# Performance work log

Hardware: AMD Instinct MI355X
Metric: run time of the kernel (lower is better)

## Reference

```python
import jax, jax.numpy as jnp
import numpy as np

NUM_STREAM = 4
SINKHORN_ITERS = 20
HC_EPS = 1e-06
NORM_EPS = 1e-06


def sinkhorn_knopps(h, iters, eps):
    # h: [B, S, ns, ns]
    h = jax.nn.softmax(h, axis=-1) + eps
    h = h / (h.sum(-2, keepdims=True) + eps)
    for _ in range(iters - 1):  # fixed small trip count (19), unrolled
        h = h / (h.sum(-1, keepdims=True) + eps)
        h = h / (h.sum(-2, keepdims=True) + eps)
    return h


def setup_inputs() -> dict:
    key = jax.random.key(0)
    k1, k2, k3, k4 = jax.random.split(key, 4)
    B, S, ns, H = 4, 2048, NUM_STREAM, 1024
    mix_hc = (2 + ns) * ns  # 24
    x = jax.random.normal(k1, (B, S, ns, H), dtype=jnp.float32)
    hc_fn = jax.random.normal(k2, (mix_hc, ns * H), dtype=jnp.float32) * 0.02
    hc_scale = jax.random.uniform(k3, (3,), dtype=jnp.float32)
    hc_base = jax.random.normal(k4, (mix_hc,), dtype=jnp.float32)
    return {"x": x, "hc_fn": hc_fn, "hc_scale": hc_scale, "hc_base": hc_base}


def reference(x, hc_fn, hc_scale, hc_base):
    B, S, ns, H = x.shape
    xf = x.reshape(B, S, ns * H).astype(jnp.float32)
    # RMSNorm stats (applied as a post-scale on the linear output, as in source)
    rsqrt = jax.lax.rsqrt(jnp.mean(jnp.square(xf), axis=-1, keepdims=True) + NORM_EPS)
    weight = jnp.einsum('bsd,md->bsm', xf, hc_fn) * rsqrt  # [B, S, mix_hc]
    h_pre = weight[..., :ns]
    h_post = weight[..., ns:2 * ns]
    h_res = weight[..., 2 * ns:].reshape(B, S, ns, ns)
    h_pre = jax.nn.sigmoid(h_pre * hc_scale[0] + hc_base[:ns][None, None, :]) + HC_EPS
    h_post = 2.0 * jax.nn.sigmoid(h_post * hc_scale[1] + hc_base[ns:2 * ns][None, None, :])
    h_res = h_res * hc_scale[2] + hc_base[2 * ns:].reshape(ns, ns)[None, None, :, :]
    h_res = sinkhorn_knopps(h_res, SINKHORN_ITERS, HC_EPS)
    xs = xf.reshape(B, S, ns, H)
    # hc_pre: mix streams into a single vector per token
    y = jnp.einsum('bsn,bsnh->bsh', h_pre, xs)  # [B, S, H]
    # hc_post: broadcast gated y back to streams + Sinkhorn-mixed residual streams
    out = h_post[..., None] * y[:, :, None, :] + jnp.einsum('bsij,bsih->bsjh', h_res, xs)
    return out.astype(x.dtype)
```

## Files before the change

kernel.cpp:

```cpp
#include <hip/hip_runtime.h>
#include <math.h>

#define NS 4
#define HDIM 1024
#define DDIM 4096
#define TOK_B 32
#define KCH 512
#define NPS 16
#define HC_EPS_F 1e-6f
#define NORM_EPS_F 1e-6f

typedef __attribute__((ext_vector_type(8))) short short8;
typedef __attribute__((ext_vector_type(4))) float f32x4;

__device__ __forceinline__ float frcp(float v) { return __builtin_amdgcn_rcpf(v); }

__device__ __forceinline__ void gload_lds16(const float* g, float* l) {
  __builtin_amdgcn_global_load_lds(
      (const __attribute__((address_space(1))) void*)g,
      (__attribute__((address_space(3))) void*)l, 16, 0, 0);
}

#define CVT_PAIR(j, f0, f1)                                                     \
  { unsigned p0 = __float_as_uint(f0), p1 = __float_as_uint(f1);                \
    H.u[j] = (p1 & 0xFFFF0000u) | (p0 >> 16);                                   \
    unsigned q0 = __float_as_uint((f0) - __uint_as_float(p0 & 0xFFFF0000u));    \
    unsigned q1 = __float_as_uint((f1) - __uint_as_float(p1 & 0xFFFF0000u));    \
    L.u[j] = (q1 & 0xFFFF0000u) | (q0 >> 16); }

__device__ __forceinline__ void cvt_hl(const float4 a, const float4 b,
                                       short8& hi, short8& lo) {
  union { unsigned u[4]; short8 s; } H, L;
  CVT_PAIR(0, a.x, a.y)
  CVT_PAIR(1, a.z, a.w)
  CVT_PAIR(2, b.x, b.y)
  CVT_PAIR(3, b.z, b.w)
  hi = H.s; lo = L.s;
}

__launch_bounds__(256, 2)
__global__ void mhc_dots_mfma(const float* __restrict__ x,
                              const float* __restrict__ hc_fn,
                              float* __restrict__ wp, int ntok) {
  __shared__ float xs[TOK_B * KCH];
  const int tid  = threadIdx.x;
  const int lane = tid & 63;
  const int wave = tid >> 6;
  const int mt = blockIdx.x >> 3;
  const int kc = blockIdx.x & 7;
  const long long tok0 = (long long)mt * TOK_B;
  const int k0 = kc * KCH;

  #pragma unroll
  for (int c = 0; c < 16; ++c) {
    const int S = c * 256 + wave * 64;
    const int t = S >> 7;
    const int b = (S & 127) + lane;
    gload_lds16(x + (tok0 + t) * DDIM + k0 + b * 4, xs + (size_t)S * 4);
  }

  const int th = wave & 1;
  const int kh = wave >> 1;
  const int row = lane & 15;
  const int ks  = lane >> 4;

  const float4* bp0 = (const float4*)(hc_fn + (long long)row * DDIM + k0 + kh * 256) + ks * 2;
  const int fr1c = (row < 8) ? (16 + row) : 23;
  const float4* bp1 = (const float4*)(hc_fn + (long long)fr1c * DDIM + k0 + kh * 256) + ks * 2;
  const bool v1 = (row < 8);
  const float4 z4 = {0.f, 0.f, 0.f, 0.f};

  f32x4 acc0 = {0.f, 0.f, 0.f, 0.f};
  f32x4 acc1 = {0.f, 0.f, 0.f, 0.f};
  float ssq = 0.f;

  float4 b00_c = bp0[0], b01_c = bp0[1];
  float4 b10_c = v1 ? bp1[0] : z4, b11_c = v1 ? bp1[1] : z4;

  __syncthreads();

  const float* a_base = xs + (size_t)(th * 16 + row) * KCH + kh * 256 + ks * 8;

  #pragma unroll
  for (int s = 0; s < 8; ++s) {
    float4 b00_n, b01_n, b10_n, b11_n;
    if (s < 7) {
      const int o = (s + 1) * 8;
      b00_n = bp0[o]; b01_n = bp0[o + 1];
      b10_n = v1 ? bp1[o] : z4; b11_n = v1 ? bp1[o + 1] : z4;
    }
    const float4 a0 = *(const float4*)(a_base + s * 32);
    const float4 a1 = *(const float4*)(a_base + s * 32 + 4);

    ssq = fmaf(a0.x, a0.x, fmaf(a0.y, a0.y, fmaf(a0.z, a0.z, fmaf(a0.w, a0.w, ssq))));
    ssq = fmaf(a1.x, a1.x, fmaf(a1.y, a1.y, fmaf(a1.z, a1.z, fmaf(a1.w, a1.w, ssq))));

    short8 ahi, alo, b0hi, b0lo, b1hi, b1lo;
    cvt_hl(a0, a1, ahi, alo);
    cvt_hl(b00_c, b01_c, b0hi, b0lo);
    cvt_hl(b10_c, b11_c, b1hi, b1lo);

    acc0 = __builtin_amdgcn_mfma_f32_16x16x32_bf16(ahi, b0hi, acc0, 0, 0, 0);
    acc1 = __builtin_amdgcn_mfma_f32_16x16x32_bf16(ahi, b1hi, acc1, 0, 0, 0);
    acc0 = __builtin_amdgcn_mfma_f32_16x16x32_bf16(ahi, b0lo, acc0, 0, 0, 0);
    acc1 = __builtin_amdgcn_mfma_f32_16x16x32_bf16(ahi, b1lo, acc1, 0, 0, 0);
    acc0 = __builtin_amdgcn_mfma_f32_16x16x32_bf16(alo, b0hi, acc0, 0, 0, 0);
    acc1 = __builtin_amdgcn_mfma_f32_16x16x32_bf16(alo, b1hi, acc1, 0, 0, 0);

    if (s < 7) {
      b00_c = b00_n; b01_c = b01_n;
      b10_c = b10_n; b11_c = b11_n;
    }
  }

  ssq += __shfl_xor(ssq, 16, 64);
  ssq += __shfl_xor(ssq, 32, 64);

  const int ps = kc * 2 + kh;
  float* wpk = wp + (long long)ps * ntok * 25;
  const long long tbase = tok0 + th * 16;
  if (lane < 16) wpk[(tbase + lane) * 25 + 24] = ssq;
  const int rq = lane >> 4;
  #pragma unroll
  for (int r = 0; r < 4; ++r)
    wpk[(tbase + rq * 4 + r) * 25 + row] = acc0[r];
  if (row < 8) {
    #pragma unroll
    for (int r = 0; r < 4; ++r)
      wpk[(tbase + rq * 4 + r) * 25 + 16 + row] = acc1[r];
  }
}

__launch_bounds__(256, 4)
__global__ void mhc_sinkhorn(const float* __restrict__ wp,
                             const float* __restrict__ hc_scale,
                             const float* __restrict__ hc_base,
                             float* __restrict__ gates, int ntok) {
  const int lane = threadIdx.x & 63;
  const int wave = threadIdx.x >> 6;
  const long long tok = (long long)blockIdx.x * 16 + wave * 4 + (lane >> 4);
  const int e = lane & 15;

  const long long kstride = (long long)ntok * 25;
  const float* b = wp + tok * 25;
  float sres = 0.f, ssq = 0.f, spre = 0.f, spost = 0.f;
  #pragma unroll
  for (int ps = 0; ps < NPS; ++ps) {
    const float* p = b + ps * kstride;
    sres += p[8 + e];
    ssq  += p[24];
    if (e < NS) { spre += p[e]; spost += p[NS + e]; }
  }

  const float rs = rsqrtf(ssq * (1.0f / DDIM) + NORM_EPS_F);
  const float s0 = hc_scale[0], s1 = hc_scale[1], s2 = hc_scale[2];

  float h = sres * rs * s2 + hc_base[8 + e];
  float mx = fmaxf(h, __shfl_xor(h, 1, 4));
  mx = fmaxf(mx, __shfl_xor(mx, 2, 4));
  float ex = expf(h - mx);
  float sm = ex + __shfl_xor(ex, 1, 4);
  sm += __shfl_xor(sm, 2, 4);
  h = ex * frcp(sm) + HC_EPS_F;
  float cs = h + __shfl_xor(h, 4, 16);
  cs += __shfl_xor(cs, 8, 16);
  h *= frcp(cs + HC_EPS_F);
  #pragma unroll 1
  for (int itn = 0; itn < 19; ++itn) {
    float rsum = h + __shfl_xor(h, 1, 4);
    rsum += __shfl_xor(rsum, 2, 4);
    h *= frcp(rsum + HC_EPS_F);
    float csum = h + __shfl_xor(h, 4, 16);
    csum += __shfl_xor(csum, 8, 16);
    h *= frcp(csum + HC_EPS_F);
  }
  float* g = gates + tok * 24;
  g[8 + e] = h;
  if (e < NS) {
    g[e] = frcp(1.0f + expf(-(spre * rs * s0 + hc_base[e]))) + HC_EPS_F;
    g[NS + e] = 2.0f * frcp(1.0f + expf(-(spost * rs * s1 + hc_base[NS + e])));
  }
}

__launch_bounds__(256, 8)
__global__ void mhc_out(const float* __restrict__ x,
                        const float* __restrict__ gates,
                        float* __restrict__ out) {
  const long long token = blockIdx.x;
  const int q = threadIdx.x;

  const float* g = gates + token * 24;
  float hp[NS], hq[NS], hr[NS][NS];
  #pragma unroll
  for (int i = 0; i < NS; ++i) {
    hp[i] = g[i];
    hq[i] = g[NS + i];
    #pragma unroll
    for (int j = 0; j < NS; ++j) hr[i][j] = g[8 + i * NS + j];
  }

  const float4* xb = (const float4*)(x + token * DDIM);
  float4 xv[NS];
  #pragma unroll
  for (int i = 0; i < NS; ++i) xv[i] = xb[i * 256 + q];

  float4 y;
  y.x = hp[0]*xv[0].x + hp[1]*xv[1].x + hp[2]*xv[2].x + hp[3]*xv[3].x;
  y.y = hp[0]*xv[0].y + hp[1]*xv[1].y + hp[2]*xv[2].y + hp[3]*xv[3].y;
  y.z = hp[0]*xv[0].z + hp[1]*xv[1].z + hp[2]*xv[2].z + hp[3]*xv[3].z;
  y.w = hp[0]*xv[0].w + hp[1]*xv[1].w + hp[2]*xv[2].w + hp[3]*xv[3].w;

  float4* ob = (float4*)(out + token * DDIM);
  #pragma unroll
  for (int n = 0; n < NS; ++n) {
    float4 o;
    o.x = hq[n]*y.x + hr[0][n]*xv[0].x + hr[1][n]*xv[1].x + hr[2][n]*xv[2].x + hr[3][n]*xv[3].x;
    o.y = hq[n]*y.y + hr[0][n]*xv[0].y + hr[1][n]*xv[1].y + hr[2][n]*xv[2].y + hr[3][n]*xv[3].y;
    o.z = hq[n]*y.z + hr[0][n]*xv[0].z + hr[1][n]*xv[1].z + hr[2][n]*xv[2].z + hr[3][n]*xv[3].z;
    o.w = hq[n]*y.w + hr[0][n]*xv[0].w + hr[1][n]*xv[1].w + hr[2][n]*xv[2].w + hr[3][n]*xv[3].w;
    ob[n * 256 + q] = o;
  }
}

extern "C" void kernel_launch(void* const* d_in, const int* in_sizes, int n_in,
                              void* d_out, int out_size, void* d_ws, size_t ws_size,
                              hipStream_t stream) {
  const float* x        = (const float*)d_in[0];
  const float* hc_fn    = (const float*)d_in[1];
  const float* hc_scale = (const float*)d_in[2];
  const float* hc_base  = (const float*)d_in[3];
  float* out = (float*)d_out;

  const int ntok = in_sizes[0] / DDIM;
  float* gates = (float*)d_ws;
  float* wp    = out;

  mhc_dots_mfma<<<(ntok / TOK_B) * 8, 256, 0, stream>>>(x, hc_fn, wp, ntok);
  mhc_sinkhorn<<<ntok / 16, 256, 0, stream>>>(wp, hc_scale, hc_base, gates, ntok);
  mhc_out<<<ntok, 256, 0, stream>>>(x, gates, out);
}
```

Baseline: 99.84 us.

## Pre-split hc_fn into bf16 hi/lo once, shrink token tile, swizzle LDS

Adds a small kernel that converts hc_fn into bf16 hi and lo arrays once per call, so the dots kernel no longer repeats that conversion per block. The dots kernel now uses 16-token tiles with four waves splitting K, which doubles the block count and the number of K partials the Sinkhorn kernel reduces (NPS 32). The LDS layout is XOR-swizzled to reduce bank conflicts. The costs are an extra launch, twice as much partial-sum traffic through the output buffer, and the converted weights stored in the output scratch area.

```diff
diff --git a/kernel.cpp b/kernel.cpp
--- a/kernel.cpp
+++ b/kernel.cpp
@@ -4,9 +4,9 @@
 #define NS 4
 #define HDIM 1024
 #define DDIM 4096
-#define TOK_B 32
+#define TOK_B 16
 #define KCH 512
-#define NPS 16
+#define NPS 32
 #define HC_EPS_F 1e-6f
 #define NORM_EPS_F 1e-6f
 
@@ -38,9 +38,26 @@
   hi = H.s; lo = L.s;
 }
 
+__launch_bounds__(256, 4)
+__global__ void mhc_convb(const float* __restrict__ hc_fn,
+                          unsigned short* __restrict__ bh,
+                          unsigned short* __restrict__ bl) {
+  const int g = blockIdx.x * 256 + threadIdx.x;
+  const float4 v = ((const float4*)hc_fn)[g];
+  ushort4 h, l;
+  unsigned p;
+  p = __float_as_uint(v.x); h.x = p >> 16; l.x = __float_as_uint(v.x - __uint_as_float(p & 0xFFFF0000u)) >> 16;
+  p = __float_as_uint(v.y); h.y = p >> 16; l.y = __float_as_uint(v.y - __uint_as_float(p & 0xFFFF0000u)) >> 16;
+  p = __float_as_uint(v.z); h.z = p >> 16; l.z = __float_as_uint(v.z - __uint_as_float(p & 0xFFFF0000u)) >> 16;
+  p = __float_as_uint(v.w); h.w = p >> 16; l.w = __float_as_uint(v.w - __uint_as_float(p & 0xFFFF0000u)) >> 16;
+  ((ushort4*)bh)[g] = h;
+  ((ushort4*)bl)[g] = l;
+}
+
 __launch_bounds__(256, 2)
 __global__ void mhc_dots_mfma(const float* __restrict__ x,
-                              const float* __restrict__ hc_fn,
+                              const unsigned short* __restrict__ bh,
+                              const unsigned short* __restrict__ bl,
                               float* __restrict__ wp, int ntok) {
   __shared__ float xs[TOK_B * KCH];
   const int tid  = threadIdx.x;
@@ -52,82 +69,86 @@
   const int k0 = kc * KCH;
 
   #pragma unroll
-  for (int c = 0; c < 16; ++c) {
+  for (int c = 0; c < 8; ++c) {
     const int S = c * 256 + wave * 64;
     const int t = S >> 7;
-    const int b = (S & 127) + lane;
-    gload_lds16(x + (tok0 + t) * DDIM + k0 + b * 4, xs + (size_t)S * 4);
-  }
-
-  const int th = wave & 1;
-  const int kh = wave >> 1;
+    const int c4src = (((wave & 1) * 64 + lane) ^ (t & 7));
+    gload_lds16(x + (tok0 + t) * DDIM + k0 + c4src * 4, xs + (size_t)S * 4);
+  }
+
+  const int kh  = wave;
   const int row = lane & 15;
   const int ks  = lane >> 4;
 
-  const float4* bp0 = (const float4*)(hc_fn + (long long)row * DDIM + k0 + kh * 256) + ks * 2;
+  const unsigned short* bp0h = bh + (long long)row * DDIM + k0 + kh * 128 + ks * 8;
+  const unsigned short* bp0l = bl + (long long)row * DDIM + k0 + kh * 128 + ks * 8;
   const int fr1c = (row < 8) ? (16 + row) : 23;
-  const float4* bp1 = (const float4*)(hc_fn + (long long)fr1c * DDIM + k0 + kh * 256) + ks * 2;
+  const unsigned short* bp1h = bh + (long long)fr1c * DDIM + k0 + kh * 128 + ks * 8;
+  const unsigned short* bp1l = bl + (long long)fr1c * DDIM + k0 + kh * 128 + ks * 8;
   const bool v1 = (row < 8);
-  const float4 z4 = {0.f, 0.f, 0.f, 0.f};
+  const short8 z8 = {0, 0, 0, 0, 0, 0, 0, 0};
 
   f32x4 acc0 = {0.f, 0.f, 0.f, 0.f};
   f32x4 acc1 = {0.f, 0.f, 0.f, 0.f};
   float ssq = 0.f;
 
-  float4 b00_c = bp0[0], b01_c = bp0[1];
-  float4 b10_c = v1 ? bp1[0] : z4, b11_c = v1 ? bp1[1] : z4;
+  short8 b0h_c = *(const short8*)bp0h;
+  short8 b0l_c = *(const short8*)bp0l;
+  short8 b1h_c = v1 ? *(const short8*)bp1h : z8;
+  short8 b1l_c = v1 ? *(const short8*)bp1l : z8;
 
   __syncthreads();
 
-  const float* a_base = xs + (size_t)(th * 16 + row) * KCH + kh * 256 + ks * 8;
-
-  #pragma unroll
-  for (int s = 0; s < 8; ++s) {
-    float4 b00_n, b01_n, b10_n, b11_n;
-    if (s < 7) {
-      const int o = (s + 1) * 8;
-      b00_n = bp0[o]; b01_n = bp0[o + 1];
-      b10_n = v1 ? bp1[o] : z4; b11_n = v1 ? bp1[o + 1] : z4;
+  const int rsw = row & 7;
+  const float* arow = xs + (size_t)row * KCH;
+
+  #pragma unroll
+  for (int s = 0; s < 4; ++s) {
+    short8 b0h_n, b0l_n, b1h_n, b1l_n;
+    if (s < 3) {
+      const int o = (s + 1) * 32;
+      b0h_n = *(const short8*)(bp0h + o);
+      b0l_n = *(const short8*)(bp0l + o);
+      b1h_n = v1 ? *(const short8*)(bp1h + o) : z8;
+      b1l_n = v1 ? *(const short8*)(bp1l + o) : z8;
     }
-    const float4 a0 = *(const float4*)(a_base + s * 32);
-    const float4 a1 = *(const float4*)(a_base + s * 32 + 4);
+    const int c4 = kh * 32 + s * 8 + ks * 2;
+    const float4 a0 = *(const float4*)(arow + (size_t)(c4 ^ rsw) * 4);
+    const float4 a1 = *(const float4*)(arow + (size_t)((c4 + 1) ^ rsw) * 4);
 
     ssq = fmaf(a0.x, a0.x, fmaf(a0.y, a0.y, fmaf(a0.z, a0.z, fmaf(a0.w, a0.w, ssq))));
     ssq = fmaf(a1.x, a1.x, fmaf(a1.y, a1.y, fmaf(a1.z, a1.z, fmaf(a1.w, a1.w, ssq))));
 
-    short8 ahi, alo, b0hi, b0lo, b1hi, b1lo;
+    short8 ahi, alo;
     cvt_hl(a0, a1, ahi, alo);
-    cvt_hl(b00_c, b01_c, b0hi, b0lo);
-    cvt_hl(b10_c, b11_c, b1hi, b1lo);
-
-    acc0 = __builtin_amdgcn_mfma_f32_16x16x32_bf16(ahi, b0hi, acc0, 0, 0, 0);
-    acc1 = __builtin_amdgcn_mfma_f32_16x16x32_bf16(ahi, b1hi, acc1, 0, 0, 0);
-    acc0 = __builtin_amdgcn_mfma_f32_16x16x32_bf16(ahi, b0lo, acc0, 0, 0, 0);
-    acc1 = __builtin_amdgcn_mfma_f32_16x16x32_bf16(ahi, b1lo, acc1, 0, 0, 0);
-    acc0 = __builtin_amdgcn_mfma_f32_16x16x32_bf16(alo, b0hi, acc0, 0, 0, 0);
-    acc1 = __builtin_amdgcn_mfma_f32_16x16x32_bf16(alo, b1hi, acc1, 0, 0, 0);
-
-    if (s < 7) {
-      b00_c = b00_n; b01_c = b01_n;
-      b10_c = b10_n; b11_c = b11_n;
+
+    acc0 = __builtin_amdgcn_mfma_f32_16x16x32_bf16(ahi, b0h_c, acc0, 0, 0, 0);
+    acc1 = __builtin_amdgcn_mfma_f32_16x16x32_bf16(ahi, b1h_c, acc1, 0, 0, 0);
+    acc0 = __builtin_amdgcn_mfma_f32_16x16x32_bf16(ahi, b0l_c, acc0, 0, 0, 0);
+    acc1 = __builtin_amdgcn_mfma_f32_16x16x32_bf16(ahi, b1l_c, acc1, 0, 0, 0);
+    acc0 = __builtin_amdgcn_mfma_f32_16x16x32_bf16(alo, b0h_c, acc0, 0, 0, 0);
+    acc1 = __builtin_amdgcn_mfma_f32_16x16x32_bf16(alo, b1h_c, acc1, 0, 0, 0);
+
+    if (s < 3) {
+      b0h_c = b0h_n; b0l_c = b0l_n;
+      b1h_c = b1h_n; b1l_c = b1l_n;
     }
   }
 
   ssq += __shfl_xor(ssq, 16, 64);
   ssq += __shfl_xor(ssq, 32, 64);
 
-  const int ps = kc * 2 + kh;
+  const int ps = kc * 4 + kh;
   float* wpk = wp + (long long)ps * ntok * 25;
-  const long long tbase = tok0 + th * 16;
-  if (lane < 16) wpk[(tbase + lane) * 25 + 24] = ssq;
+  if (lane < 16) wpk[(tok0 + lane) * 25 + 24] = ssq;
   const int rq = lane >> 4;
   #pragma unroll
   for (int r = 0; r < 4; ++r)
-    wpk[(tbase + rq * 4 + r) * 25 + row] = acc0[r];
+    wpk[(tok0 + rq * 4 + r) * 25 + row] = acc0[r];
   if (row < 8) {
     #pragma unroll
     for (int r = 0; r < 4; ++r)
-      wpk[(tbase + rq * 4 + r) * 25 + 16 + row] = acc1[r];
+      wpk[(tok0 + rq * 4 + r) * 25 + 16 + row] = acc1[r];
   }
 }
 
@@ -144,7 +165,7 @@
   const long long kstride = (long long)ntok * 25;
   const float* b = wp + tok * 25;
   float sres = 0.f, ssq = 0.f, spre = 0.f, spost = 0.f;
-  #pragma unroll
+  #pragma unroll 4
   for (int ps = 0; ps < NPS; ++ps) {
     const float* p = b + ps * kstride;
     sres += p[8 + e];
@@ -233,9 +254,13 @@
 
   const int ntok = in_sizes[0] / DDIM;
   float* gates = (float*)d_ws;
-  float* wp    = out;
-
-  mhc_dots_mfma<<<(ntok / TOK_B) * 8, 256, 0, stream>>>(x, hc_fn, wp, ntok);
+
+  float* wp = out;
+  unsigned short* bh = (unsigned short*)(out + (size_t)NPS * ntok * 25);
+  unsigned short* bl = bh + 24 * DDIM;
+
+  mhc_convb<<<(24 * DDIM / 4) / 256, 256, 0, stream>>>(hc_fn, bh, bl);
+  mhc_dots_mfma<<<(ntok / TOK_B) * 8, 256, 0, stream>>>(x, bh, bl, wp, ntok);
   mhc_sinkhorn<<<ntok / 16, 256, 0, stream>>>(wp, hc_scale, hc_base, gates, ntok);
   mhc_out<<<ntok, 256, 0, stream>>>(x, gates, out);
 }
```

Measured after the change: 100.2 us. About the same (+0.3%).
